# Kernel tuning notes

Measured on AMD Instinct MI355X. Metric: run time of the kernel, lower is better.

Reference implementation:

```python
import jax, jax.numpy as jnp
import numpy as np

B, S, D = 4, 2048, 768

def setup_inputs() -> dict:
    key = jax.random.key(0)
    ks = jax.random.split(key, 7)
    scale = 1.0 / np.sqrt(D)
    x = jax.random.normal(ks[0], (B, S, D), dtype=jnp.float32)
    Wq = jax.random.uniform(ks[1], (D, D), jnp.float32, -scale, scale)
    bq = jax.random.uniform(ks[2], (D,), jnp.float32, -scale, scale)
    Wk = jax.random.uniform(ks[3], (D, D), jnp.float32, -scale, scale)
    bk = jax.random.uniform(ks[4], (D,), jnp.float32, -scale, scale)
    Wv = jax.random.uniform(ks[5], (D, D), jnp.float32, -scale, scale)
    bv = jax.random.uniform(ks[6], (D,), jnp.float32, -scale, scale)
    return {"x": x, "Wq": Wq, "bq": bq, "Wk": Wk, "bk": bk, "Wv": Wv, "bv": bv}

def reference(x, Wq, bq, Wk, bk, Wv, bv):
    d = x.shape[-1]
    q = jnp.einsum('bsd,de->bse', x, Wq) + bq
    k = jnp.einsum('bsd,de->bse', x, Wk) + bk
    v = jnp.einsum('bsd,de->bse', x, Wv) + bv
    scores = jnp.einsum('bqd,bkd->bqk', q, k) / jnp.sqrt(jnp.asarray(d, x.dtype))
    attn = jax.nn.softmax(scores, axis=-1)  # [B,S,S]
    return jnp.einsum('bqk,bkd->bqd', attn, v)
```

## Files before the change

### kernel.cpp

```cpp
#include <hip/hip_runtime.h>
#include <hip/hip_bf16.h>


typedef __attribute__((ext_vector_type(8))) short short8;
typedef __attribute__((ext_vector_type(4))) short short4v;
typedef __attribute__((ext_vector_type(4))) float float4v;

static constexpr int B_ = 4, S_ = 2048, D_ = 768;
static constexpr int MS = B_ * S_;

__device__ inline short f2bf(float f) {
  __hip_bfloat16 h = __float2bfloat16(f);
  union { __hip_bfloat16 h; short s; } u; u.h = h; return u.s;
}
__device__ inline float bf2f(short s) {
  union { unsigned int u; float f; } c;
  c.u = ((unsigned int)(unsigned short)s) << 16; return c.f;
}

typedef const __attribute__((address_space(1))) unsigned int g_u32;
typedef __attribute__((address_space(3))) unsigned int l_u32;

__device__ __forceinline__ void glds16(const short* g, short* l) {
  __builtin_amdgcn_global_load_lds((g_u32*)g, (l_u32*)l, 16, 0, 0);
}

__global__ __launch_bounds__(256)
void cast_f32_bf16(const float* __restrict__ x, short* __restrict__ y, int n) {
  int i = (blockIdx.x * 256 + threadIdx.x) * 4;
  if (i + 3 < n) {
    float4v v = *(const float4v*)(x + i);
    short4v o;
    o.x = f2bf(v.x); o.y = f2bf(v.y); o.z = f2bf(v.z); o.w = f2bf(v.w);
    *(short4v*)(y + i) = o;
  }
}

__global__ void transpose_cast_w(const float* __restrict__ W0, const float* __restrict__ W1,
                                 const float* __restrict__ W2,
                                 short* __restrict__ T0, short* __restrict__ T1,
                                 short* __restrict__ T2) {
  const float* W = blockIdx.z == 0 ? W0 : (blockIdx.z == 1 ? W1 : W2);
  short* T = blockIdx.z == 0 ? T0 : (blockIdx.z == 1 ? T1 : T2);
  __shared__ float tile[32][33];
  int bx = blockIdx.x * 32, by = blockIdx.y * 32;
  int tx = threadIdx.x, ty = threadIdx.y;
  for (int r = ty; r < 32; r += 8)
    tile[r][tx] = W[(by + r) * D_ + bx + tx];
  __syncthreads();
  for (int r = ty; r < 32; r += 8)
    T[(bx + r) * D_ + by + tx] = f2bf(tile[tx][r]);
}

template<int EPI, int TM, int TN>
__global__ __launch_bounds__(256)
void gemm_bt(const short* __restrict__ A, const short* __restrict__ Bt,
             void* __restrict__ C0v, void* __restrict__ C1v,
             const float* __restrict__ bias0, const float* __restrict__ bias1,
             const float* __restrict__ linv,
             int K, int lda, int ldb, int ldc,
             long sA, long sB, long sC, float scale) {
  constexpr int BMv = TM * 32, BNv = TN * 32;
  const int b = blockIdx.z;
  A += (long)b * sA;
  Bt += (long)b * sB;
  float* Cf = (float*)C0v + (long)b * sC;
  short* Cs = (short*)C0v + (long)b * sC;
  short* Cs1 = (short*)C1v;
  const float* linv_b = linv + (long)b * S_;

  __shared__ short As[BMv * 64];
  __shared__ short Bs[BNv * 64];

  const int t = threadIdx.x;
  const int wave = t >> 6, lane = t & 63;
  const int lane16 = lane & 15, q = lane >> 4;
  const int m0 = blockIdx.y * BMv, n0 = blockIdx.x * BNv;
  const int wm = (wave >> 1) * (TM * 16), wn = (wave & 1) * (TN * 16);
  const int rsub = lane >> 3;
  const int g = (lane & 7) ^ rsub;

  float4v acc[TM][TN];
#pragma unroll
  for (int i = 0; i < TM; i++)
#pragma unroll
    for (int j = 0; j < TN; j++) acc[i][j] = {0.f, 0.f, 0.f, 0.f};

  for (int k0 = 0; k0 < K; k0 += 64) {
#pragma unroll
    for (int i = wave; i < BMv / 8; i += 4)
      glds16(A + (long)(m0 + i * 8 + rsub) * lda + k0 + g * 8, &As[i * 512]);
#pragma unroll
    for (int i = wave; i < BNv / 8; i += 4)
      glds16(Bt + (long)(n0 + i * 8 + rsub) * ldb + k0 + g * 8, &Bs[i * 512]);
    __syncthreads();

    short8 af[2][TM], bfr[2][TN];
#pragma unroll
    for (int s = 0; s < 2; s++) {
#pragma unroll
      for (int i = 0; i < TM; i++) {
        int R = wm + i * 16 + lane16;
        af[s][i] = *(const short8*)&As[R * 64 + (((s * 4 + q) ^ (R & 7)) * 8)];
      }
#pragma unroll
      for (int j = 0; j < TN; j++) {
        int R = wn + j * 16 + lane16;
        bfr[s][j] = *(const short8*)&Bs[R * 64 + (((s * 4 + q) ^ (R & 7)) * 8)];
      }
    }
    __syncthreads();

#pragma unroll
    for (int s = 0; s < 2; s++)
#pragma unroll
      for (int i = 0; i < TM; i++)
#pragma unroll
        for (int j = 0; j < TN; j++)
          acc[i][j] = __builtin_amdgcn_mfma_f32_16x16x32_bf16(af[s][i], bfr[s][j], acc[i][j], 0, 0, 0);
  }

#pragma unroll
  for (int i = 0; i < TM; i++) {
    int mrow = m0 + wm + i * 16 + q * 4;
#pragma unroll
    for (int j = 0; j < TN; j++) {
      int ncol = n0 + wn + j * 16 + lane16;
#pragma unroll
      for (int rr = 0; rr < 4; rr++) {
        float v = acc[i][j][rr];
        if (EPI == 0) {
          if (ncol < 768) Cs [(long)(mrow + rr) * 768 + ncol]       = f2bf(v + bias0[ncol]);
          else            Cs1[(long)(mrow + rr) * 768 + ncol - 768] = f2bf(v + bias1[ncol - 768]);
        } else if (EPI == 1) {
          Cs[(long)(mrow + rr) * ldc + ncol] = f2bf(v + bias0[mrow + rr]);
        } else if (EPI == 2) {
          Cs[(long)(mrow + rr) * ldc + ncol] = f2bf(__expf(v * scale));
        } else {
          Cf[(long)(mrow + rr) * ldc + ncol] = v * linv_b[mrow + rr];
        }
      }
    }
  }
}

__global__ __launch_bounds__(256)
void rowsum_inv(const short* __restrict__ Es, float* __restrict__ linv) {
  long row = blockIdx.x;
  const short* pr = Es + row * (long)S_;
  int t = threadIdx.x;
  int wave = t >> 6, lane = t & 63;

  short8 v = *(const short8*)(pr + t * 8);
  float s = 0.f;
#pragma unroll
  for (int i = 0; i < 8; i++) s += bf2f(v[i]);
  for (int off = 1; off < 64; off <<= 1) s += __shfl_xor(s, off);
  __shared__ float reds[4];
  if (lane == 0) reds[wave] = s;
  __syncthreads();
  if (t == 0) linv[row] = 1.0f / (reds[0] + reds[1] + reds[2] + reds[3]);
}

extern "C" void kernel_launch(void* const* d_in, const int* in_sizes, int n_in,
                              void* d_out, int out_size, void* d_ws, size_t ws_size,
                              hipStream_t stream) {
  const float* x  = (const float*)d_in[0];
  const float* Wq = (const float*)d_in[1];
  const float* bq = (const float*)d_in[2];
  const float* Wk = (const float*)d_in[3];
  const float* bk = (const float*)d_in[4];
  const float* Wv = (const float*)d_in[5];
  const float* bv = (const float*)d_in[6];
  float* out = (float*)d_out;

  short* Xb  = (short*)d_ws;
  short* WqT = Xb + (long)MS * D_;
  short* WkT = WqT + (long)D_ * D_;
  short* WvT = WkT + (long)D_ * D_;
  short* Qb  = WvT + (long)D_ * D_;
  short* Kb  = Qb + (long)MS * D_;
  short* Vt  = Kb + (long)MS * D_;
  short* Es  = Vt + (long)MS * D_;
  float* linv = (float*)(Es + (long)B_ * S_ * S_);

  cast_f32_bf16<<<(MS * D_) / 1024, 256, 0, stream>>>(x, Xb, MS * D_);
  transpose_cast_w<<<dim3(24, 24, 3), dim3(32, 8), 0, stream>>>(Wq, Wk, Wv, WqT, WkT, WvT);

  gemm_bt<0, 2, 4><<<dim3(1536 / 128, MS / 64, 1), 256, 0, stream>>>(
      Xb, WqT, Qb, Kb, bq, bk, nullptr, D_, D_, D_, D_, 0, 0, 0, 1.0f);
  gemm_bt<1, 2, 4><<<dim3(MS / 128, D_ / 64, 1), 256, 0, stream>>>(
      WvT, Xb, Vt, nullptr, bv, nullptr, nullptr, D_, D_, D_, MS, 0, 0, 0, 1.0f);
  gemm_bt<2, 4, 4><<<dim3(S_ / 128, S_ / 128, B_), 256, 0, stream>>>(
      Qb, Kb, Es, nullptr, nullptr, nullptr, nullptr, D_, D_, D_, S_,
      (long)S_ * D_, (long)S_ * D_, (long)S_ * S_, 1.0f / sqrtf((float)D_));
  rowsum_inv<<<MS, 256, 0, stream>>>(Es, linv);
  gemm_bt<3, 2, 4><<<dim3(D_ / 128, S_ / 64, B_), 256, 0, stream>>>(
      Es, Vt, out, nullptr, nullptr, nullptr, linv, S_, S_, MS, D_,
      (long)S_ * S_, (long)S_, (long)S_ * D_, 1.0f);
}
```

Before: 226.1 us.

## Fuse QKV projections, fold softmax rowsum into exp epilogue, prefetch next K-tile

Merges the Q/K and V projection GEMMs into one launch over all 2304 output columns, writing V transposed with vector stores. Computes softmax row sums inside the exp epilogue using shuffle reductions and atomicAdd into a zeroed buffer, removing the separate rowsum kernel and its extra pass over the score matrix. The GEMM loop now issues the next tile's global-to-LDS loads right after the fragment reads, so they overlap with the MFMAs. In exchange it adds a memset, atomic contention on the row sums, and a division per row in the final epilogue.

```diff
diff --git a/kernel.cpp b/kernel.cpp
--- a/kernel.cpp
+++ b/kernel.cpp
@@ -55,9 +55,9 @@
 template<int EPI, int TM, int TN>
 __global__ __launch_bounds__(256)
 void gemm_bt(const short* __restrict__ A, const short* __restrict__ Bt,
-             void* __restrict__ C0v, void* __restrict__ C1v,
+             void* __restrict__ C0v, short* __restrict__ C1, short* __restrict__ C2,
              const float* __restrict__ bias0, const float* __restrict__ bias1,
-             const float* __restrict__ linv,
+             const float* __restrict__ bias2, float* __restrict__ rowsum,
              int K, int lda, int ldb, int ldc,
              long sA, long sB, long sC, float scale) {
   constexpr int BMv = TM * 32, BNv = TN * 32;
@@ -66,8 +66,7 @@
   Bt += (long)b * sB;
   float* Cf = (float*)C0v + (long)b * sC;
   short* Cs = (short*)C0v + (long)b * sC;
-  short* Cs1 = (short*)C1v;
-  const float* linv_b = linv + (long)b * S_;
+  float* rowsum_b = rowsum + (long)b * S_;
 
   __shared__ short As[BMv * 64];
   __shared__ short Bs[BNv * 64];
@@ -80,6 +79,17 @@
   const int rsub = lane >> 3;
   const int g = (lane & 7) ^ rsub;
 
+  auto stage = [&](int kk) {
+#pragma unroll
+    for (int i = wave; i < BMv / 8; i += 4)
+      glds16(A + (long)(m0 + i * 8 + rsub) * lda + kk + g * 8, &As[i * 512]);
+#pragma unroll
+    for (int i = wave; i < BNv / 8; i += 4)
+      glds16(Bt + (long)(n0 + i * 8 + rsub) * ldb + kk + g * 8, &Bs[i * 512]);
+  };
+
+  stage(0);
+
   float4v acc[TM][TN];
 #pragma unroll
   for (int i = 0; i < TM; i++)
@@ -87,12 +97,6 @@
     for (int j = 0; j < TN; j++) acc[i][j] = {0.f, 0.f, 0.f, 0.f};
 
   for (int k0 = 0; k0 < K; k0 += 64) {
-#pragma unroll
-    for (int i = wave; i < BMv / 8; i += 4)
-      glds16(A + (long)(m0 + i * 8 + rsub) * lda + k0 + g * 8, &As[i * 512]);
-#pragma unroll
-    for (int i = wave; i < BNv / 8; i += 4)
-      glds16(Bt + (long)(n0 + i * 8 + rsub) * ldb + k0 + g * 8, &Bs[i * 512]);
     __syncthreads();
 
     short8 af[2][TM], bfr[2][TN];
@@ -111,6 +115,8 @@
     }
     __syncthreads();
 
+    if (k0 + 64 < K) stage(k0 + 64);
+
 #pragma unroll
     for (int s = 0; s < 2; s++)
 #pragma unroll
@@ -123,43 +129,52 @@
 #pragma unroll
   for (int i = 0; i < TM; i++) {
     int mrow = m0 + wm + i * 16 + q * 4;
-#pragma unroll
-    for (int j = 0; j < TN; j++) {
-      int ncol = n0 + wn + j * 16 + lane16;
+    if (EPI == 0) {
+#pragma unroll
+      for (int j = 0; j < TN; j++) {
+        int ncol = n0 + wn + j * 16 + lane16;
+        if (ncol < 1536) {
+          short* dst = ncol < 768 ? Cs : C1;
+          const float* bs = ncol < 768 ? bias0 : bias1;
+          int c = ncol < 768 ? ncol : ncol - 768;
+#pragma unroll
+          for (int rr = 0; rr < 4; rr++)
+            dst[(long)(mrow + rr) * 768 + c] = f2bf(acc[i][j][rr] + bs[c]);
+        } else {
+          int e = ncol - 1536;
+          float bv = bias2[e];
+          short4v o;
+#pragma unroll
+          for (int rr = 0; rr < 4; rr++) o[rr] = f2bf(acc[i][j][rr] + bv);
+          *(short4v*)&C2[(long)e * MS + mrow] = o;
+        }
+      }
+    } else if (EPI == 2) {
 #pragma unroll
       for (int rr = 0; rr < 4; rr++) {
-        float v = acc[i][j][rr];
-        if (EPI == 0) {
-          if (ncol < 768) Cs [(long)(mrow + rr) * 768 + ncol]       = f2bf(v + bias0[ncol]);
-          else            Cs1[(long)(mrow + rr) * 768 + ncol - 768] = f2bf(v + bias1[ncol - 768]);
-        } else if (EPI == 1) {
-          Cs[(long)(mrow + rr) * ldc + ncol] = f2bf(v + bias0[mrow + rr]);
-        } else if (EPI == 2) {
-          Cs[(long)(mrow + rr) * ldc + ncol] = f2bf(__expf(v * scale));
-        } else {
-          Cf[(long)(mrow + rr) * ldc + ncol] = v * linv_b[mrow + rr];
+        float rsumv = 0.f;
+#pragma unroll
+        for (int j = 0; j < TN; j++) {
+          int ncol = n0 + wn + j * 16 + lane16;
+          short sv = f2bf(__expf(acc[i][j][rr] * scale));
+          Cs[(long)(mrow + rr) * ldc + ncol] = sv;
+          rsumv += bf2f(sv);
+        }
+        for (int off = 1; off < 16; off <<= 1) rsumv += __shfl_xor(rsumv, off);
+        if (lane16 == 0) atomicAdd(&rowsum_b[mrow + rr], rsumv);
+      }
+    } else {
+#pragma unroll
+      for (int rr = 0; rr < 4; rr++) {
+        float inv = 1.0f / rowsum_b[mrow + rr];
+#pragma unroll
+        for (int j = 0; j < TN; j++) {
+          int ncol = n0 + wn + j * 16 + lane16;
+          Cf[(long)(mrow + rr) * ldc + ncol] = acc[i][j][rr] * inv;
         }
       }
     }
   }
-}
-
-__global__ __launch_bounds__(256)
-void rowsum_inv(const short* __restrict__ Es, float* __restrict__ linv) {
-  long row = blockIdx.x;
-  const short* pr = Es + row * (long)S_;
-  int t = threadIdx.x;
-  int wave = t >> 6, lane = t & 63;
-
-  short8 v = *(const short8*)(pr + t * 8);
-  float s = 0.f;
-#pragma unroll
-  for (int i = 0; i < 8; i++) s += bf2f(v[i]);
-  for (int off = 1; off < 64; off <<= 1) s += __shfl_xor(s, off);
-  __shared__ float reds[4];
-  if (lane == 0) reds[wave] = s;
-  __syncthreads();
-  if (t == 0) linv[row] = 1.0f / (reds[0] + reds[1] + reds[2] + reds[3]);
 }
 
 extern "C" void kernel_launch(void* const* d_in, const int* in_sizes, int n_in,
@@ -182,20 +197,21 @@
   short* Kb  = Qb + (long)MS * D_;
   short* Vt  = Kb + (long)MS * D_;
   short* Es  = Vt + (long)MS * D_;
-  float* linv = (float*)(Es + (long)B_ * S_ * S_);
-
+  float* rowsum = (float*)(Es + (long)B_ * S_ * S_);
+
+  hipMemsetAsync(rowsum, 0, MS * sizeof(float), stream);
   cast_f32_bf16<<<(MS * D_) / 1024, 256, 0, stream>>>(x, Xb, MS * D_);
   transpose_cast_w<<<dim3(24, 24, 3), dim3(32, 8), 0, stream>>>(Wq, Wk, Wv, WqT, WkT, WvT);
 
-  gemm_bt<0, 2, 4><<<dim3(1536 / 128, MS / 64, 1), 256, 0, stream>>>(
-      Xb, WqT, Qb, Kb, bq, bk, nullptr, D_, D_, D_, D_, 0, 0, 0, 1.0f);
-  gemm_bt<1, 2, 4><<<dim3(MS / 128, D_ / 64, 1), 256, 0, stream>>>(
-      WvT, Xb, Vt, nullptr, bv, nullptr, nullptr, D_, D_, D_, MS, 0, 0, 0, 1.0f);
+  gemm_bt<0, 2, 4><<<dim3(2304 / 128, MS / 64, 1), 256, 0, stream>>>(
+      Xb, WqT, Qb, Kb, Vt, bq, bk, bv, nullptr,
+      D_, D_, D_, D_, 0, 0, 0, 1.0f);
   gemm_bt<2, 4, 4><<<dim3(S_ / 128, S_ / 128, B_), 256, 0, stream>>>(
-      Qb, Kb, Es, nullptr, nullptr, nullptr, nullptr, D_, D_, D_, S_,
+      Qb, Kb, Es, nullptr, nullptr, nullptr, nullptr, nullptr, rowsum,
+      D_, D_, D_, S_,
       (long)S_ * D_, (long)S_ * D_, (long)S_ * S_, 1.0f / sqrtf((float)D_));
-  rowsum_inv<<<MS, 256, 0, stream>>>(Es, linv);
   gemm_bt<3, 2, 4><<<dim3(D_ / 128, S_ / 64, B_), 256, 0, stream>>>(
-      Es, Vt, out, nullptr, nullptr, nullptr, linv, S_, S_, MS, D_,
+      Es, Vt, out, nullptr, nullptr, nullptr, nullptr, nullptr, rowsum,
+      S_, S_, MS, D_,
       (long)S_ * S_, (long)S_, (long)S_ * D_, 1.0f);
 }
```

New measurement: 213.3 us. -5.7%, faster.
